# Kernel optimization log

Measured on AMD Instinct MI355X. Metric: run time of the kernel, lower is better.

The kernel has to match this reference:

```python
import jax, jax.numpy as jnp
import numpy as np

MAX_FRAMES = 12
TOPK = 49
NUM_SAMPLES = 256
SIGMA = 0.05
LN_EPS = 1e-5


def setup_inputs() -> dict:
    key = jax.random.key(0)
    ks = jax.random.split(key, 6)
    B, MF, N, D = 8, MAX_FRAMES, 197, 512
    x = jax.random.normal(ks[0], (B, MF * N, D), dtype=jnp.float32)
    noise = jax.random.normal(ks[1], (B * MF, NUM_SAMPLES, N - 1), dtype=jnp.float32)
    ln_gamma = jnp.ones((D,), jnp.float32)
    ln_beta = jnp.zeros((D,), jnp.float32)
    w_in = jax.random.normal(ks[2], (D, D // 2), dtype=jnp.float32) * 0.02
    w1 = jax.random.normal(ks[3], (D, D // 2), dtype=jnp.float32) * 0.02
    w2 = jax.random.normal(ks[4], (D // 2, 1), dtype=jnp.float32) * 0.02
    return {"x": x, "noise": noise, "ln_gamma": ln_gamma, "ln_beta": ln_beta,
            "w_in": w_in, "w1": w1, "w2": w2}


def reference(x, noise, ln_gamma, ln_beta, w_in, w1, w2):
    B, L, D = x.shape
    N = L // MAX_FRAMES
    xf = x.reshape(B * MAX_FRAMES, N, D)          # (b, N, D)

    # PredictorLG: LayerNorm -> Linear -> GELU (torch GELU is exact erf)
    mu = xf.mean(-1, keepdims=True)
    var = xf.var(-1, keepdims=True)               # biased, matches torch LayerNorm
    hn = (xf - mu) * jax.lax.rsqrt(var + LN_EPS) * ln_gamma + ln_beta
    h = jax.nn.gelu(hn @ w_in, approximate=False)  # (b, N, D/2)
    # concat local features with broadcast global (cls-token) features
    g = jnp.broadcast_to(h[:, :1, :], h.shape)
    cat = jnp.concatenate([h, g], axis=-1)         # (b, N, D)
    score = jnp.tanh(jax.nn.gelu(cat @ w1, approximate=False) @ w2)[..., 0]  # (b, N)

    sp = score[:, 1:]                              # (b, d) spatial scores, d = N-1
    b_eff, ns, d = noise.shape
    pert = sp[:, None, :] + noise * SIGMA          # (b, ns, d)

    # top-k set per sample; sorted ascending (matches torch sort of topk indices)
    order = jnp.argsort(-pert, axis=-1)            # descending by value
    top_sorted = jnp.sort(order[..., :TOPK], axis=-1)  # (b, ns, k)

    # mean of one-hots == scatter-add counts / num_samples (avoids one-hot blowup)
    bi = jnp.arange(b_eff)[:, None, None]
    pos = jnp.arange(TOPK)[None, None, :]
    ind = jnp.zeros((b_eff, TOPK, d), x.dtype).at[bi, pos, top_sorted].add(1.0) / ns

    cls_feat = xf[:, :1, :]                        # (b, 1, D)
    spat_feat = xf[:, 1:, :]                       # (b, d, D)
    sel = jnp.einsum('bkl,bld->bkd', ind, spat_feat)  # (b, k, D)
    out = jnp.concatenate([cls_feat, sel], axis=1)    # (b, 1+k, D)
    return out.reshape(B, MAX_FRAMES * (1 + TOPK), D)
```

## Files before the change

kernel.cpp:

```cpp
#include <hip/hip_runtime.h>
#include <math.h>

#define NFRAME 96
#define NTOK   197
#define NSPAT  196
#define DIM    512
#define DH     256
#define NSAMP  256
#define KSEL   49
#define SIG    0.05f
#define MPAD   208
#define MTOT   (NFRAME * MPAD)

typedef unsigned short u16;
typedef __attribute__((ext_vector_type(8))) short bf16x8;
typedef __attribute__((ext_vector_type(4))) float f32x4;

__device__ __forceinline__ float gelu_exact(float v) {
    return 0.5f * v * (1.0f + erff(v * 0.70710678118654752440f));
}
__device__ __forceinline__ unsigned bf16_rne(float f) {
    unsigned u = __float_as_uint(f);
    return (u + 0x7fffu + ((u >> 16) & 1u)) >> 16;
}
__device__ __forceinline__ float bf16_to_f(unsigned h) {
    return __uint_as_float(h << 16);
}

__global__ __launch_bounds__(256) void k0_wsplit(
    const float* __restrict__ w_in, const float* __restrict__ w1,
    u16* __restrict__ wiT_hi, u16* __restrict__ wiT_lo,
    u16* __restrict__ w1T_hi, u16* __restrict__ w1T_lo)
{
    const int n = blockIdx.x & 255, which = blockIdx.x >> 8;
    const float* w = which ? w1 : w_in;
    u16* th = which ? w1T_hi : wiT_hi;
    u16* tl = which ? w1T_lo : wiT_lo;
    for (int k = threadIdx.x; k < DIM; k += 256) {
        float v = w[(size_t)k * DH + n];
        unsigned hi = bf16_rne(v);
        unsigned lo = bf16_rne(v - bf16_to_f(hi));
        th[(size_t)n * DIM + k] = (u16)hi;
        tl[(size_t)n * DIM + k] = (u16)lo;
    }
}

__global__ __launch_bounds__(256) void k0_ln_split(
    const float* __restrict__ x, const float* __restrict__ gamma,
    const float* __restrict__ beta,
    u16* __restrict__ xs_hi, u16* __restrict__ xs_lo)
{
    const int row  = blockIdx.x * 4 + (threadIdx.x >> 6);
    const int lane = threadIdx.x & 63;
    const int f = row / MPAD;
    int rr = row - f * MPAD; if (rr > NTOK - 1) rr = NTOK - 1;
    const float* xr = x + ((size_t)f * NTOK + rr) * DIM + lane * 8;
    float4 a = *(const float4*)xr, b4 = *(const float4*)(xr + 4);
    float e[8] = {a.x, a.y, a.z, a.w, b4.x, b4.y, b4.z, b4.w};
    float s = 0.f, sq = 0.f;
    #pragma unroll
    for (int j = 0; j < 8; ++j) { s += e[j]; sq += e[j] * e[j]; }
    #pragma unroll
    for (int o = 32; o > 0; o >>= 1) {
        s  += __shfl_xor(s,  o, 64);
        sq += __shfl_xor(sq, o, 64);
    }
    const float mu  = s * (1.f / 512.f);
    const float var = sq * (1.f / 512.f) - mu * mu;
    const float rs  = 1.f / sqrtf(var + 1e-5f);

    const float* gp = gamma + lane * 8;
    const float* bp = beta + lane * 8;
    float4 g0 = *(const float4*)gp, g1 = *(const float4*)(gp + 4);
    float4 b0 = *(const float4*)bp, b1 = *(const float4*)(bp + 4);
    float gg[8] = {g0.x, g0.y, g0.z, g0.w, g1.x, g1.y, g1.z, g1.w};
    float bt[8] = {b0.x, b0.y, b0.z, b0.w, b1.x, b1.y, b1.z, b1.w};

    unsigned hw[4], lw[4];
    #pragma unroll
    for (int p = 0; p < 4; ++p) {
        float s0 = rs * gg[2*p],   s1 = rs * gg[2*p+1];
        float v0 = e[2*p]   * s0 + (bt[2*p]   - mu * s0);
        float v1 = e[2*p+1] * s1 + (bt[2*p+1] - mu * s1);
        unsigned h0 = bf16_rne(v0), h1 = bf16_rne(v1);
        float l0 = v0 - bf16_to_f(h0), l1 = v1 - bf16_to_f(h1);
        hw[p] = h0 | (h1 << 16);
        lw[p] = bf16_rne(l0) | (bf16_rne(l1) << 16);
    }
    size_t off = (size_t)row * DIM + lane * 8;
    *(uint4*)(xs_hi + off) = make_uint4(hw[0], hw[1], hw[2], hw[3]);
    *(uint4*)(xs_lo + off) = make_uint4(lw[0], lw[1], lw[2], lw[3]);
}

#define LDG 40
__global__ __launch_bounds__(256, 4) void k1_gemm1(
    const u16* __restrict__ xs_hi, const u16* __restrict__ xs_lo,
    const u16* __restrict__ wiT_hi, const u16* __restrict__ wiT_lo,
    u16* __restrict__ h_hi, u16* __restrict__ h_lo)
{
    __shared__ u16 Ah[128][LDG], Al[128][LDG], Bh[64][LDG], Bl[64][LDG];
    const int t = threadIdx.x, lane = t & 63, wv = t >> 6;
    const int Mb = blockIdx.x >> 2, Nb = blockIdx.x & 3;
    const int R0 = Mb * 128, N0 = Nb * 64;
    const int wm = wv >> 1, wn = wv & 1;
    const int m15 = lane & 15, q = lane >> 4;

    f32x4 acc[4][2];
    #pragma unroll
    for (int i = 0; i < 4; ++i)
        #pragma unroll
        for (int j = 0; j < 2; ++j)
            acc[i][j] = (f32x4){0.f, 0.f, 0.f, 0.f};

    const int ar = t >> 1, as = (t & 1) * 16;
    const int br = t >> 2, bs = (t & 3) * 8;
    const size_t abase = (size_t)(R0 + ar) * DIM + as;
    const size_t bbase = (size_t)(N0 + br) * DIM + bs;

    for (int k0 = 0; k0 < DIM; k0 += 32) {
        __syncthreads();
        *(uint4*)&Ah[ar][as]     = *(const uint4*)(xs_hi + abase + k0);
        *(uint4*)&Ah[ar][as + 8] = *(const uint4*)(xs_hi + abase + k0 + 8);
        *(uint4*)&Al[ar][as]     = *(const uint4*)(xs_lo + abase + k0);
        *(uint4*)&Al[ar][as + 8] = *(const uint4*)(xs_lo + abase + k0 + 8);
        *(uint4*)&Bh[br][bs]     = *(const uint4*)(wiT_hi + bbase + k0);
        *(uint4*)&Bl[br][bs]     = *(const uint4*)(wiT_lo + bbase + k0);
        __syncthreads();

        const int ko = q * 8;
        bf16x8 ah[4], al[4], bh[2], bl[2];
        #pragma unroll
        for (int i = 0; i < 4; ++i) {
            ah[i] = *(const bf16x8*)&Ah[wm*64 + i*16 + m15][ko];
            al[i] = *(const bf16x8*)&Al[wm*64 + i*16 + m15][ko];
        }
        #pragma unroll
        for (int i = 0; i < 2; ++i) {
            bh[i] = *(const bf16x8*)&Bh[wn*32 + i*16 + m15][ko];
            bl[i] = *(const bf16x8*)&Bl[wn*32 + i*16 + m15][ko];
        }
        #pragma unroll
        for (int mt = 0; mt < 4; ++mt)
            #pragma unroll
            for (int nt = 0; nt < 2; ++nt) {
                f32x4 c = acc[mt][nt];
                c = __builtin_amdgcn_mfma_f32_16x16x32_bf16(ah[mt], bh[nt], c, 0, 0, 0);
                c = __builtin_amdgcn_mfma_f32_16x16x32_bf16(al[mt], bh[nt], c, 0, 0, 0);
                c = __builtin_amdgcn_mfma_f32_16x16x32_bf16(ah[mt], bl[nt], c, 0, 0, 0);
                acc[mt][nt] = c;
            }
    }

    #pragma unroll
    for (int mt = 0; mt < 4; ++mt)
        #pragma unroll
        for (int nt = 0; nt < 2; ++nt)
            #pragma unroll
            for (int reg = 0; reg < 4; ++reg) {
                int r = R0 + wm*64 + mt*16 + q*4 + reg;
                int c = N0 + wn*32 + nt*16 + m15;
                float v = gelu_exact(acc[mt][nt][reg]);
                unsigned hb = bf16_rne(v);
                unsigned lb = bf16_rne(v - bf16_to_f(hb));
                size_t off = (size_t)r * DH + c;
                h_hi[off] = (u16)hb;
                h_lo[off] = (u16)lb;
            }
}

__global__ __launch_bounds__(256, 4) void k1_gemm2(
    const u16* __restrict__ h_hi, const u16* __restrict__ h_lo,
    const u16* __restrict__ w1T_hi, const u16* __restrict__ w1T_lo,
    const float* __restrict__ w2, float* __restrict__ s_half)
{
    __shared__ u16 Ah[64][LDG], Al[64][LDG], Bh[128][LDG], Bl[128][LDG];
    __shared__ float red[2][2][32];
    const int t = threadIdx.x, lane = t & 63, wv = t >> 6;
    const int Mb = blockIdx.x >> 1, Nb = blockIdx.x & 1;
    const int R0 = Mb * 64, N0 = Nb * 128;
    const int wm = wv >> 1, wn = wv & 1;
    const int m15 = lane & 15, q = lane >> 4;

    f32x4 acc[2][4];
    #pragma unroll
    for (int i = 0; i < 2; ++i)
        #pragma unroll
        for (int j = 0; j < 4; ++j)
            acc[i][j] = (f32x4){0.f, 0.f, 0.f, 0.f};

    const int ar = t >> 2, as = (t & 3) * 8;
    const int agrow = R0 + ar;
    const size_t arow_off = (size_t)agrow * DH;
    const size_t g0_off   = (size_t)((agrow / MPAD) * MPAD) * DH;
    const int br = t >> 1, bs = (t & 1) * 16;
    const size_t bbase = (size_t)(N0 + br) * DIM + bs;

    for (int k0 = 0; k0 < DIM; k0 += 32) {
        __syncthreads();
        {
            size_t src = (k0 < DH) ? (arow_off + k0 + as)
                                   : (g0_off + (k0 - DH) + as);
            *(uint4*)&Ah[ar][as] = *(const uint4*)(h_hi + src);
            *(uint4*)&Al[ar][as] = *(const uint4*)(h_lo + src);
        }
        *(uint4*)&Bh[br][bs]     = *(const uint4*)(w1T_hi + bbase + k0);
        *(uint4*)&Bh[br][bs + 8] = *(const uint4*)(w1T_hi + bbase + k0 + 8);
        *(uint4*)&Bl[br][bs]     = *(const uint4*)(w1T_lo + bbase + k0);
        *(uint4*)&Bl[br][bs + 8] = *(const uint4*)(w1T_lo + bbase + k0 + 8);
        __syncthreads();

        const int ko = q * 8;
        bf16x8 ah[2], al[2], bh[4], bl[4];
        #pragma unroll
        for (int i = 0; i < 2; ++i) {
            ah[i] = *(const bf16x8*)&Ah[wm*32 + i*16 + m15][ko];
            al[i] = *(const bf16x8*)&Al[wm*32 + i*16 + m15][ko];
        }
        #pragma unroll
        for (int i = 0; i < 4; ++i) {
            bh[i] = *(const bf16x8*)&Bh[wn*64 + i*16 + m15][ko];
            bl[i] = *(const bf16x8*)&Bl[wn*64 + i*16 + m15][ko];
        }
        #pragma unroll
        for (int mt = 0; mt < 2; ++mt)
            #pragma unroll
            for (int nt = 0; nt < 4; ++nt) {
                f32x4 c = acc[mt][nt];
                c = __builtin_amdgcn_mfma_f32_16x16x32_bf16(ah[mt], bh[nt], c, 0, 0, 0);
                c = __builtin_amdgcn_mfma_f32_16x16x32_bf16(al[mt], bh[nt], c, 0, 0, 0);
                c = __builtin_amdgcn_mfma_f32_16x16x32_bf16(ah[mt], bl[nt], c, 0, 0, 0);
                acc[mt][nt] = c;
            }
    }

    float w2v[4];
    #pragma unroll
    for (int nt = 0; nt < 4; ++nt) w2v[nt] = w2[N0 + wn*64 + nt*16 + m15];
    #pragma unroll
    for (int mt = 0; mt < 2; ++mt)
        #pragma unroll
        for (int reg = 0; reg < 4; ++reg) {
            float s = 0.f;
            #pragma unroll
            for (int nt = 0; nt < 4; ++nt)
                s += gelu_exact(acc[mt][nt][reg]) * w2v[nt];
            #pragma unroll
            for (int o = 1; o <= 8; o <<= 1)
                s += __shfl_xor(s, o, 64);
            if (m15 == 0)
                red[wn][wm][mt*16 + q*4 + reg] = s;
        }
    __syncthreads();
    if (t < 64) {
        int wmj = t >> 5, rl = t & 31;
        float sv = red[0][wmj][rl] + red[1][wmj][rl];
        s_half[(size_t)Nb * MTOT + R0 + t] = sv;
    }
}

__global__ __launch_bounds__(1024) void k2_select(
    const float* __restrict__ s_half, const float* __restrict__ noise,
    int* __restrict__ hist2)
{
    const int fb   = blockIdx.x;
    const int f    = fb >> 1;
    const int half = fb & 1;
    const int t    = threadIdx.x;
    const int lane = t & 63;
    const int wv   = t >> 6;

    __shared__ int hist_s[KSEL * NSPAT];
    for (int i = t; i < KSEL * NSPAT; i += 1024) hist_s[i] = 0;

    const float* sA = s_half;
    const float* sB = s_half + MTOT;
    float spv[4];
    #pragma unroll
    for (int j = 0; j < 4; ++j) {
        int l = lane + 64 * j;
        if (l < NSPAT) {
            size_t idx = (size_t)f * MPAD + 1 + l;
            spv[j] = tanhf(sA[idx] + sB[idx]);
        } else spv[j] = 0.f;
    }
    __syncthreads();

    const unsigned long long lmask = (1ull << lane) - 1ull;

    for (int si = 0; si < 8; ++si) {
        const int s = half * 128 + wv * 8 + si;
        const float* nz = noise + ((size_t)f * NSAMP + s) * NSPAT;
        unsigned key[4];
        #pragma unroll
        for (int j = 0; j < 4; ++j) {
            int l = lane + 64 * j;
            if (l < NSPAT) {
                float p = spv[j] + nz[l] * SIG;
                unsigned u = __float_as_uint(p);
                key[j] = (u & 0x80000000u) ? ~u : (u | 0x80000000u);
            } else {
                key[j] = 0u;
            }
        }

        unsigned ans = 0u;
        for (int bit = 31; bit >= 0; --bit) {
            unsigned cand = ans | (1u << bit);
            int cnt = 0;
            #pragma unroll
            for (int j = 0; j < 4; ++j)
                cnt += __popcll(__ballot(key[j] >= cand));
            if (cnt >= KSEL) ans = cand;
        }

        unsigned long long eq[4];
        int cgt = 0;
        #pragma unroll
        for (int j = 0; j < 4; ++j) {
            cgt += __popcll(__ballot(key[j] > ans));
            eq[j] = __ballot(key[j] == ans);
        }
        const int quota = KSEL - cgt;
        int eqpre[4]; { int run = 0;
            #pragma unroll
            for (int j = 0; j < 4; ++j) { eqpre[j] = run; run += __popcll(eq[j]); } }

        int pre = 0;
        #pragma unroll
        for (int j = 0; j < 4; ++j) {
            bool iseq = (key[j] == ans);
            int trk = eqpre[j] + __popcll(eq[j] & lmask);
            bool selj = (key[j] > ans) || (iseq && trk < quota);
            unsigned long long sb = __ballot(selj);
            int rk = pre + __popcll(sb & lmask);
            if (selj)
                atomicAdd(&hist_s[rk * NSPAT + lane + 64 * j], 1);
            pre += __popcll(sb);
        }
    }

    __syncthreads();
    int* hb = hist2 + (size_t)fb * (KSEL * NSPAT);
    for (int i = t; i < KSEL * NSPAT; i += 1024)
        hb[i] = hist_s[i];
}

__global__ __launch_bounds__(256) void k3_output(
    const float* __restrict__ x, const int* __restrict__ hist2,
    float* __restrict__ out)
{
    const int b  = blockIdx.x >> 2;
    const int ds = blockIdx.x & 3;
    const int d0 = ds * 128;
    const int t  = threadIdx.x;
    const int tdc = t & 31;
    const int tk  = t >> 5;

    __shared__ float hist_s[NSPAT * KSEL + 8];

    const int* h0 = hist2 + (size_t)(2 * b) * (KSEL * NSPAT);
    const int* h1 = h0 + KSEL * NSPAT;
    for (int i = t; i < KSEL * NSPAT; i += 256) {
        int k = i / NSPAT;
        int l = i - k * NSPAT;
        hist_s[l * KSEL + k] = (float)(h0[i] + h1[i]);
    }
    if (t < 128)
        out[(size_t)b * 50 * DIM + d0 + t] = x[(size_t)b * NTOK * DIM + d0 + t];
    __syncthreads();

    const float* xs = x + ((size_t)b * NTOK + 1) * DIM + d0 + tdc * 4;
    float4 acc[7];
    #pragma unroll
    for (int i = 0; i < 7; ++i) acc[i] = make_float4(0.f, 0.f, 0.f, 0.f);

    #pragma unroll 2
    for (int l = 0; l < NSPAT; ++l) {
        float4 v = *(const float4*)(xs + (size_t)l * DIM);
        const float* hl = &hist_s[l * KSEL + tk];
        #pragma unroll
        for (int i = 0; i < 7; ++i) {
            float w = hl[8 * i];
            acc[i].x += w * v.x; acc[i].y += w * v.y;
            acc[i].z += w * v.z; acc[i].w += w * v.w;
        }
    }

    const float inv = 1.f / 256.f;
    #pragma unroll
    for (int i = 0; i < 7; ++i) {
        int k = tk + 8 * i;
        if (k < KSEL) {
            float4 o = make_float4(acc[i].x * inv, acc[i].y * inv,
                                   acc[i].z * inv, acc[i].w * inv);
            *(float4*)&out[((size_t)b * 50 + 1 + k) * DIM + d0 + tdc * 4] = o;
        }
    }
}

extern "C" void kernel_launch(void* const* d_in, const int* in_sizes, int n_in,
                              void* d_out, int out_size, void* d_ws, size_t ws_size,
                              hipStream_t stream)
{
    const float* x     = (const float*)d_in[0];
    const float* noise = (const float*)d_in[1];
    const float* gamma = (const float*)d_in[2];
    const float* beta  = (const float*)d_in[3];
    const float* w_in  = (const float*)d_in[4];
    const float* w1    = (const float*)d_in[5];
    const float* w2    = (const float*)d_in[6];
    float* out = (float*)d_out;

    char* ws = (char*)d_ws;
    int*   hist2   = (int*)  (ws + 0);
    float* s_half  = (float*)(ws + 7375872);
    u16*   wiT_hi  = (u16*)  (ws + 7535616);
    u16*   wiT_lo  = (u16*)  (ws + 7797760);
    u16*   w1T_hi  = (u16*)  (ws + 8059904);
    u16*   w1T_lo  = (u16*)  (ws + 8322048);
    u16*   h_hi    = (u16*)  (ws + 8584192);
    u16*   h_lo    = (u16*)  (ws + 18807808);
    u16*   xs_hi   = (u16*)  (ws + 29031424);
    u16*   xs_lo   = (u16*)  (ws + 49478656);

    k0_wsplit<<<512, 256, 0, stream>>>(w_in, w1, wiT_hi, wiT_lo, w1T_hi, w1T_lo);
    k0_ln_split<<<MTOT / 4, 256, 0, stream>>>(x, gamma, beta, xs_hi, xs_lo);
    k1_gemm1<<<(MTOT / 128) * 4, 256, 0, stream>>>(xs_hi, xs_lo, wiT_hi, wiT_lo,
                                                   h_hi, h_lo);
    k1_gemm2<<<(MTOT / 64) * 2, 256, 0, stream>>>(h_hi, h_lo, w1T_hi, w1T_lo,
                                                  w2, s_half);
    k2_select<<<NFRAME * 2, 1024, 0, stream>>>(s_half, noise, hist2);
    k3_output<<<NFRAME * 4, 256, 0, stream>>>(x, hist2, out);
}
```

Measured before the change: 248.0 us.

## Prefetch next k-tile into registers, swizzle GEMM blocks per XCD, merge prep kernels

Both GEMM kernels now load the next k-slice of A and B from global memory into registers while the current slice is consumed, overlapping global latency with MFMA work. Block indices are remapped so consecutive tiles land on the same XCD, improving L2 reuse of shared rows and weights. The weight-split and layernorm-split kernels are fused into one launch to save launch overhead. Extra live registers may reduce occupancy.

Result: faster. 234.1 us (-5.6%).

```diff
diff --git a/kernel.cpp b/kernel.cpp
--- a/kernel.cpp
+++ b/kernel.cpp
@@ -27,30 +27,29 @@
     return __uint_as_float(h << 16);
 }
 
-__global__ __launch_bounds__(256) void k0_wsplit(
+__global__ __launch_bounds__(256) void k0_prep(
+    const float* __restrict__ x, const float* __restrict__ gamma,
+    const float* __restrict__ beta,
     const float* __restrict__ w_in, const float* __restrict__ w1,
     u16* __restrict__ wiT_hi, u16* __restrict__ wiT_lo,
-    u16* __restrict__ w1T_hi, u16* __restrict__ w1T_lo)
-{
-    const int n = blockIdx.x & 255, which = blockIdx.x >> 8;
-    const float* w = which ? w1 : w_in;
-    u16* th = which ? w1T_hi : wiT_hi;
-    u16* tl = which ? w1T_lo : wiT_lo;
-    for (int k = threadIdx.x; k < DIM; k += 256) {
-        float v = w[(size_t)k * DH + n];
-        unsigned hi = bf16_rne(v);
-        unsigned lo = bf16_rne(v - bf16_to_f(hi));
-        th[(size_t)n * DIM + k] = (u16)hi;
-        tl[(size_t)n * DIM + k] = (u16)lo;
-    }
-}
-
-__global__ __launch_bounds__(256) void k0_ln_split(
-    const float* __restrict__ x, const float* __restrict__ gamma,
-    const float* __restrict__ beta,
+    u16* __restrict__ w1T_hi, u16* __restrict__ w1T_lo,
     u16* __restrict__ xs_hi, u16* __restrict__ xs_lo)
 {
-    const int row  = blockIdx.x * 4 + (threadIdx.x >> 6);
+    if (blockIdx.x < 512) {
+        const int n = blockIdx.x & 255, which = blockIdx.x >> 8;
+        const float* w = which ? w1 : w_in;
+        u16* th = which ? w1T_hi : wiT_hi;
+        u16* tl = which ? w1T_lo : wiT_lo;
+        for (int k = threadIdx.x; k < DIM; k += 256) {
+            float v = w[(size_t)k * DH + n];
+            unsigned hi = bf16_rne(v);
+            unsigned lo = bf16_rne(v - bf16_to_f(hi));
+            th[(size_t)n * DIM + k] = (u16)hi;
+            tl[(size_t)n * DIM + k] = (u16)lo;
+        }
+        return;
+    }
+    const int row  = (blockIdx.x - 512) * 4 + (threadIdx.x >> 6);
     const int lane = threadIdx.x & 63;
     const int f = row / MPAD;
     int rr = row - f * MPAD; if (rr > NTOK - 1) rr = NTOK - 1;
@@ -100,7 +99,8 @@
 {
     __shared__ u16 Ah[128][LDG], Al[128][LDG], Bh[64][LDG], Bl[64][LDG];
     const int t = threadIdx.x, lane = t & 63, wv = t >> 6;
-    const int Mb = blockIdx.x >> 2, Nb = blockIdx.x & 3;
+    const int linear = (blockIdx.x & 7) * 78 + (blockIdx.x >> 3);
+    const int Mb = linear >> 2, Nb = linear & 3;
     const int R0 = Mb * 128, N0 = Nb * 64;
     const int wm = wv >> 1, wn = wv & 1;
     const int m15 = lane & 15, q = lane >> 4;
@@ -117,14 +117,29 @@
     const size_t abase = (size_t)(R0 + ar) * DIM + as;
     const size_t bbase = (size_t)(N0 + br) * DIM + bs;
 
+    uint4 pAh0 = *(const uint4*)(xs_hi + abase);
+    uint4 pAh1 = *(const uint4*)(xs_hi + abase + 8);
+    uint4 pAl0 = *(const uint4*)(xs_lo + abase);
+    uint4 pAl1 = *(const uint4*)(xs_lo + abase + 8);
+    uint4 pBh  = *(const uint4*)(wiT_hi + bbase);
+    uint4 pBl  = *(const uint4*)(wiT_lo + bbase);
+
     for (int k0 = 0; k0 < DIM; k0 += 32) {
         __syncthreads();
-        *(uint4*)&Ah[ar][as]     = *(const uint4*)(xs_hi + abase + k0);
-        *(uint4*)&Ah[ar][as + 8] = *(const uint4*)(xs_hi + abase + k0 + 8);
-        *(uint4*)&Al[ar][as]     = *(const uint4*)(xs_lo + abase + k0);
-        *(uint4*)&Al[ar][as + 8] = *(const uint4*)(xs_lo + abase + k0 + 8);
-        *(uint4*)&Bh[br][bs]     = *(const uint4*)(wiT_hi + bbase + k0);
-        *(uint4*)&Bl[br][bs]     = *(const uint4*)(wiT_lo + bbase + k0);
+        *(uint4*)&Ah[ar][as]     = pAh0;
+        *(uint4*)&Ah[ar][as + 8] = pAh1;
+        *(uint4*)&Al[ar][as]     = pAl0;
+        *(uint4*)&Al[ar][as + 8] = pAl1;
+        *(uint4*)&Bh[br][bs]     = pBh;
+        *(uint4*)&Bl[br][bs]     = pBl;
+        if (k0 + 32 < DIM) {
+            pAh0 = *(const uint4*)(xs_hi + abase + k0 + 32);
+            pAh1 = *(const uint4*)(xs_hi + abase + k0 + 40);
+            pAl0 = *(const uint4*)(xs_lo + abase + k0 + 32);
+            pAl1 = *(const uint4*)(xs_lo + abase + k0 + 40);
+            pBh  = *(const uint4*)(wiT_hi + bbase + k0 + 32);
+            pBl  = *(const uint4*)(wiT_lo + bbase + k0 + 32);
+        }
         __syncthreads();
 
         const int ko = q * 8;
@@ -176,7 +191,8 @@
     __shared__ u16 Ah[64][LDG], Al[64][LDG], Bh[128][LDG], Bl[128][LDG];
     __shared__ float red[2][2][32];
     const int t = threadIdx.x, lane = t & 63, wv = t >> 6;
-    const int Mb = blockIdx.x >> 1, Nb = blockIdx.x & 1;
+    const int linear = (blockIdx.x & 7) * 78 + (blockIdx.x >> 3);
+    const int Mb = linear >> 1, Nb = linear & 1;
     const int R0 = Mb * 64, N0 = Nb * 128;
     const int wm = wv >> 1, wn = wv & 1;
     const int m15 = lane & 15, q = lane >> 4;
@@ -195,18 +211,34 @@
     const int br = t >> 1, bs = (t & 1) * 16;
     const size_t bbase = (size_t)(N0 + br) * DIM + bs;
 
+    auto asrc = [&](int k0) -> size_t {
+        return (k0 < DH) ? (arow_off + k0 + as) : (g0_off + (k0 - DH) + as);
+    };
+
+    uint4 pAh = *(const uint4*)(h_hi + asrc(0));
+    uint4 pAl = *(const uint4*)(h_lo + asrc(0));
+    uint4 pBh0 = *(const uint4*)(w1T_hi + bbase);
+    uint4 pBh1 = *(const uint4*)(w1T_hi + bbase + 8);
+    uint4 pBl0 = *(const uint4*)(w1T_lo + bbase);
+    uint4 pBl1 = *(const uint4*)(w1T_lo + bbase + 8);
+
     for (int k0 = 0; k0 < DIM; k0 += 32) {
         __syncthreads();
-        {
-            size_t src = (k0 < DH) ? (arow_off + k0 + as)
-                                   : (g0_off + (k0 - DH) + as);
-            *(uint4*)&Ah[ar][as] = *(const uint4*)(h_hi + src);
-            *(uint4*)&Al[ar][as] = *(const uint4*)(h_lo + src);
-        }
-        *(uint4*)&Bh[br][bs]     = *(const uint4*)(w1T_hi + bbase + k0);
-        *(uint4*)&Bh[br][bs + 8] = *(const uint4*)(w1T_hi + bbase + k0 + 8);
-        *(uint4*)&Bl[br][bs]     = *(const uint4*)(w1T_lo + bbase + k0);
-        *(uint4*)&Bl[br][bs + 8] = *(const uint4*)(w1T_lo + bbase + k0 + 8);
+        *(uint4*)&Ah[ar][as]     = pAh;
+        *(uint4*)&Al[ar][as]     = pAl;
+        *(uint4*)&Bh[br][bs]     = pBh0;
+        *(uint4*)&Bh[br][bs + 8] = pBh1;
+        *(uint4*)&Bl[br][bs]     = pBl0;
+        *(uint4*)&Bl[br][bs + 8] = pBl1;
+        if (k0 + 32 < DIM) {
+            size_t srcn = asrc(k0 + 32);
+            pAh  = *(const uint4*)(h_hi + srcn);
+            pAl  = *(const uint4*)(h_lo + srcn);
+            pBh0 = *(const uint4*)(w1T_hi + bbase + k0 + 32);
+            pBh1 = *(const uint4*)(w1T_hi + bbase + k0 + 40);
+            pBl0 = *(const uint4*)(w1T_lo + bbase + k0 + 32);
+            pBl1 = *(const uint4*)(w1T_lo + bbase + k0 + 40);
+        }
         __syncthreads();
 
         const int ko = q * 8;
@@ -423,8 +455,9 @@
     u16*   xs_hi   = (u16*)  (ws + 29031424);
     u16*   xs_lo   = (u16*)  (ws + 49478656);
 
-    k0_wsplit<<<512, 256, 0, stream>>>(w_in, w1, wiT_hi, wiT_lo, w1T_hi, w1T_lo);
-    k0_ln_split<<<MTOT / 4, 256, 0, stream>>>(x, gamma, beta, xs_hi, xs_lo);
+    k0_prep<<<512 + MTOT / 4, 256, 0, stream>>>(x, gamma, beta, w_in, w1,
+                                                wiT_hi, wiT_lo, w1T_hi, w1T_lo,
+                                                xs_hi, xs_lo);
     k1_gemm1<<<(MTOT / 128) * 4, 256, 0, stream>>>(xs_hi, xs_lo, wiT_hi, wiT_lo,
                                                    h_hi, h_lo);
     k1_gemm2<<<(MTOT / 64) * 2, 256, 0, stream>>>(h_hi, h_lo, w1T_hi, w1T_lo,
```
